# Kernel tuning notes

Hardware: AMD Instinct MI355X
Metric: run time of the kernel (lower is better)

## Reference

```python
import jax, jax.numpy as jnp
import numpy as np

M, IN, OUT = 4096, 4096, 16384

def setup_inputs() -> dict:
    key = jax.random.key(0)
    k1, k2, k3, k4 = jax.random.split(key, 4)
    x = jax.random.normal(k1, (M, IN), dtype=jnp.float32)
    weight = jax.random.randint(k2, (OUT, IN), -127, 127, dtype=jnp.int32).astype(jnp.int8)
    scale = jax.random.uniform(k3, (OUT, 1), dtype=jnp.float32) * 0.01 + 1e-4
    bias = jax.random.normal(k4, (OUT,), dtype=jnp.float32)
    return {"x": x, "weight": weight, "scale": scale, "bias": bias}

def reference(x, weight, scale, bias):
    # Dequantize int8 weights on the fly: [out, in]
    w = weight.astype(x.dtype) * scale
    # F.linear: x @ w.T + bias  -> [M, out]
    return jnp.einsum('mi,oi->mo', x, w) + bias
```

## Files before the change

kernel.cpp:

```cpp
#include <hip/hip_runtime.h>
#include <hip/hip_bf16.h>

#define M_DIM 4096
#define K_DIM 4096
#define N_DIM 16384
#define BM 256
#define BN 256
#define BKB 128
#define NT (K_DIM / BKB)
#define HALF_B 16384
#define BUF_B  (4 * HALF_B)
#define LDS_BYTES (2 * BUF_B)

using i32x4 = __attribute__((ext_vector_type(4))) int;

__global__ void cvt_w_kernel(const int* __restrict__ w,
                             signed char* __restrict__ o, int n) {
    int tid = blockIdx.x * blockDim.x + threadIdx.x;
    int stride = gridDim.x * blockDim.x;
    for (int base = tid * 16; base < n; base += stride * 16) {
        int4 a = *reinterpret_cast<const int4*>(w + base);
        int4 b = *reinterpret_cast<const int4*>(w + base + 4);
        int4 c = *reinterpret_cast<const int4*>(w + base + 8);
        int4 d = *reinterpret_cast<const int4*>(w + base + 12);
        int4 p;
        p.x = (a.x & 255) | ((a.y & 255) << 8) | ((a.z & 255) << 16) | (a.w << 24);
        p.y = (b.x & 255) | ((b.y & 255) << 8) | ((b.z & 255) << 16) | (b.w << 24);
        p.z = (c.x & 255) | ((c.y & 255) << 8) | ((c.z & 255) << 16) | (c.w << 24);
        p.w = (d.x & 255) | ((d.y & 255) << 8) | ((d.z & 255) << 16) | (d.w << 24);
        *reinterpret_cast<int4*>(o + base) = p;
    }
}

__global__ __launch_bounds__(256) void quant_x_kernel(
    const float* __restrict__ x, signed char* __restrict__ q,
    float* __restrict__ xs) {
    int row = blockIdx.x;
    int tid = threadIdx.x;
    const float* xr = x + (size_t)row * K_DIM + tid * 16;
    float4 v0 = *reinterpret_cast<const float4*>(xr + 0);
    float4 v1 = *reinterpret_cast<const float4*>(xr + 4);
    float4 v2 = *reinterpret_cast<const float4*>(xr + 8);
    float4 v3 = *reinterpret_cast<const float4*>(xr + 12);
    float f[16] = {v0.x, v0.y, v0.z, v0.w, v1.x, v1.y, v1.z, v1.w,
                   v2.x, v2.y, v2.z, v2.w, v3.x, v3.y, v3.z, v3.w};
    float m = 0.f;
    #pragma unroll
    for (int i = 0; i < 16; ++i) m = fmaxf(m, fabsf(f[i]));
    #pragma unroll
    for (int off = 32; off > 0; off >>= 1) m = fmaxf(m, __shfl_xor(m, off));
    __shared__ float red[4];
    if ((tid & 63) == 0) red[tid >> 6] = m;
    __syncthreads();
    m = fmaxf(fmaxf(red[0], red[1]), fmaxf(red[2], red[3]));
    float inv = (m > 0.f) ? 127.0f / m : 0.f;
    if (tid == 0) xs[row] = (m > 0.f) ? m / 127.0f : 0.f;
    int b[16];
    #pragma unroll
    for (int i = 0; i < 16; ++i) {
        float t = f[i] * inv;
        t = fminf(fmaxf(t, -127.f), 127.f);
        b[i] = (int)__builtin_rintf(t);
    }
    int4 p;
    p.x = (b[0] & 255) | ((b[1] & 255) << 8) | ((b[2] & 255) << 16) | (b[3] << 24);
    p.y = (b[4] & 255) | ((b[5] & 255) << 8) | ((b[6] & 255) << 16) | (b[7] << 24);
    p.z = (b[8] & 255) | ((b[9] & 255) << 8) | ((b[10] & 255) << 16) | (b[11] << 24);
    p.w = (b[12] & 255) | ((b[13] & 255) << 8) | ((b[14] & 255) << 16) | (b[15] << 24);
    *reinterpret_cast<int4*>(q + (size_t)row * K_DIM + tid * 16) = p;
}

#define FENCE() asm volatile("" ::: "memory")
#define BARRIER() do { FENCE(); __builtin_amdgcn_s_barrier(); FENCE(); } while (0)

#define READ_A(AH)                                                        \
  do { _Pragma("unroll") for (int mi = 0; mi < 4; ++mi) {                 \
    int hr = wm * 64 + mi * 16 + l15;                                     \
    const signed char* hb = lb + (AH) * HALF_B + hr * BKB;                \
    _Pragma("unroll") for (int kk = 0; kk < 2; ++kk)                      \
      af[mi][kk] = *reinterpret_cast<const i32x4*>(                       \
          hb + (((kk * 4 + lg) ^ (hr & 7)) * 16));                        \
  } } while (0)

#define READ_B(DST, BG)                                                   \
  do { _Pragma("unroll") for (int ni = 0; ni < 2; ++ni) {                 \
    int hr = wn * 32 + ni * 16 + l15;                                     \
    const signed char* hb = lb + (2 + (BG)) * HALF_B + hr * BKB;          \
    _Pragma("unroll") for (int kk = 0; kk < 2; ++kk)                      \
      DST[ni][kk] = *reinterpret_cast<const i32x4*>(                      \
          hb + (((kk * 4 + lg) ^ (hr & 7)) * 16));                        \
  } } while (0)

#define MFMA16(BSRC, AH, BG)                                              \
  do { __builtin_amdgcn_s_setprio(1);                                     \
    _Pragma("unroll") for (int kk = 0; kk < 2; ++kk)                      \
      _Pragma("unroll") for (int mi = 0; mi < 4; ++mi)                    \
        _Pragma("unroll") for (int ni = 0; ni < 2; ++ni)                  \
          acc[AH][BG][mi][ni] = __builtin_amdgcn_mfma_i32_16x16x64_i8(    \
              af[mi][kk], BSRC[ni][kk], acc[AH][BG][mi][ni], 0, 0, 0);    \
    __builtin_amdgcn_s_setprio(0);                                        \
  } while (0)

__global__ __launch_bounds__(512, 2) void gemm_kernel(
    const signed char* __restrict__ A,
    const signed char* __restrict__ B,
    const float* __restrict__ scale,
    const float* __restrict__ xs,
    const float* __restrict__ bias,
    float* __restrict__ C)
{
    extern __shared__ signed char lds[];

    const int nwg = (M_DIM / BM) * (N_DIM / BN);
    const int cpx = nwg / 8;
    int bid = blockIdx.x;
    int swz = (bid & 7) * cpx + (bid >> 3);
    const int ntn = N_DIM / BN;
    int tm = swz / ntn;
    int tn = swz % ntn;

    int tid  = threadIdx.x;
    int lane = tid & 63;
    int wid  = tid >> 6;
    int wm   = wid >> 2;
    int wn   = wid & 3;
    int l15  = lane & 15;
    int lg   = lane >> 4;

    const signed char* Ab = A + (size_t)tm * BM * K_DIM;
    const signed char* Bb = B + (size_t)tn * BN * K_DIM;

    auto STAGE = [&](int buf, int half, int t) {
        const signed char* gbase = (half < 2)
            ? Ab + (size_t)(half * 128) * K_DIM
            : Bb + (size_t)((half - 2) * 128) * K_DIM;
        signed char* dbase = lds + buf * BUF_B + half * HALF_B;
        #pragma unroll
        for (int i = 0; i < 2; ++i) {
            int flat = i * 512 + tid;
            int row = flat >> 3, ch = flat & 7;
            const signed char* src =
                gbase + (size_t)row * K_DIM + t * BKB + ((ch ^ (row & 7)) * 16);
            __builtin_amdgcn_global_load_lds(
                (const __attribute__((address_space(1))) unsigned int*)src,
                (__attribute__((address_space(3))) unsigned int*)(dbase + flat * 16),
                16, 0, 0);
        }
    };

    i32x4 acc[2][2][4][2];
    #pragma unroll
    for (int a0 = 0; a0 < 2; ++a0)
      #pragma unroll
      for (int g0 = 0; g0 < 2; ++g0)
        #pragma unroll
        for (int mi = 0; mi < 4; ++mi)
          #pragma unroll
          for (int ni = 0; ni < 2; ++ni)
            acc[a0][g0][mi][ni] = (i32x4){0, 0, 0, 0};

    i32x4 af[4][2], b0[2][2], b1[2][2];

    STAGE(0, 0, 0);
    STAGE(0, 2, 0);
    STAGE(0, 3, 0);
    STAGE(0, 1, 0);
    STAGE(1, 0, 1);
    STAGE(1, 3, 1);
    asm volatile("s_waitcnt vmcnt(4)" ::: "memory");

    for (int t = 0; t < NT; ++t) {
        const signed char* lb = lds + (t & 1) * BUF_B;
        const bool s1 = (t + 1) < NT;
        const bool s2 = (t + 2) < NT;

        BARRIER();
        if (s1) STAGE((t + 1) & 1, 1, t + 1);
        READ_A(0);
        READ_B(b0, 0);
        MFMA16(b0, 0, 0);
        if (s1) STAGE((t + 1) & 1, 2, t + 1);
        READ_B(b1, 1);
        MFMA16(b1, 0, 1);
        BARRIER();
        if (s2) STAGE(t & 1, 0, t + 2);
        READ_A(1);
        MFMA16(b1, 1, 1);
        if (s2) STAGE(t & 1, 3, t + 2);
        MFMA16(b0, 1, 0);
        if (s2) asm volatile("s_waitcnt vmcnt(4)" ::: "memory");
        else    asm volatile("s_waitcnt vmcnt(0)" ::: "memory");
    }

    #pragma unroll
    for (int AH = 0; AH < 2; ++AH)
      #pragma unroll
      for (int BG = 0; BG < 2; ++BG)
        #pragma unroll
        for (int ni = 0; ni < 2; ++ni) {
            int col = tn * BN + BG * 128 + wn * 32 + ni * 16 + l15;
            float s = scale[col];
            float b = bias[col];
            #pragma unroll
            for (int mi = 0; mi < 4; ++mi) {
                int row0 = tm * BM + AH * 128 + wm * 64 + mi * 16 + lg * 4;
                float4 x4 = *reinterpret_cast<const float4*>(xs + row0);
                float xv[4] = {x4.x, x4.y, x4.z, x4.w};
                #pragma unroll
                for (int r = 0; r < 4; ++r)
                    C[(size_t)(row0 + r) * N_DIM + col] =
                        (float)acc[AH][BG][mi][ni][r] * (s * xv[r]) + b;
            }
        }
}

__global__ void naive_kernel(const float* __restrict__ x,
                             const int* __restrict__ w,
                             const float* __restrict__ scale,
                             const float* __restrict__ bias,
                             float* __restrict__ out) {
    long long idx = (long long)blockIdx.x * blockDim.x + threadIdx.x;
    long long total = (long long)M_DIM * N_DIM;
    if (idx >= total) return;
    int m = (int)(idx / N_DIM);
    int o = (int)(idx % N_DIM);
    const float* xr = x + (size_t)m * K_DIM;
    const int* wr = w + (size_t)o * K_DIM;
    float sum = 0.f;
    for (int k = 0; k < K_DIM; ++k) sum += xr[k] * (float)wr[k];
    out[idx] = sum * scale[o] + bias[o];
}

extern "C" void kernel_launch(void* const* d_in, const int* in_sizes, int n_in,
                              void* d_out, int out_size, void* d_ws, size_t ws_size,
                              hipStream_t stream)
{
    const float* x     = (const float*)d_in[0];
    const int*   w     = (const int*)d_in[1];
    const float* scale = (const float*)d_in[2];
    const float* bias  = (const float*)d_in[3];
    float*       out   = (float*)d_out;

    const size_t needW = (size_t)N_DIM * K_DIM;
    const size_t needX = (size_t)M_DIM * K_DIM;
    const size_t needS = (size_t)M_DIM * sizeof(float);

    if (ws_size >= needW + needX + needS) {
        signed char* Wq = (signed char*)d_ws;
        signed char* Xq = (signed char*)((char*)d_ws + needW);
        float*       xs = (float*)((char*)d_ws + needW + needX);
        hipLaunchKernelGGL(cvt_w_kernel, dim3(2048), dim3(256), 0, stream,
                           w, Wq, N_DIM * K_DIM);
        hipLaunchKernelGGL(quant_x_kernel, dim3(M_DIM), dim3(256), 0, stream,
                           x, Xq, xs);
        hipLaunchKernelGGL(gemm_kernel, dim3((M_DIM / BM) * (N_DIM / BN)), dim3(512),
                           LDS_BYTES, stream, Xq, Wq, scale, xs, bias, out);
    } else {
        long long total = (long long)M_DIM * N_DIM;
        int blocks = (int)((total + 255) / 256);
        hipLaunchKernelGGL(naive_kernel, dim3(blocks), dim3(256), 0, stream,
                           x, w, scale, bias, out);
    }
}
```

Baseline: 351.7 us.

## Pre-swizzle weights into MFMA fragment layout and load B directly to registers

The weight conversion kernel now writes int8 weights in a fragment-major layout matching the 16x16x64 MFMA B operand, so each wave loads its B fragments straight from global memory into registers instead of staging through LDS. LDS holds only the A tile now (double buffered), which halves LDS use and removes the B ds_reads. The main loop is restructured into a two-tile unrolled body with register double-buffering of B fragments and a full vmcnt(0) wait plus barrier each tile. The trade-off is that B is no longer shared across waves through LDS, so each wave issues redundant global/L2 reads of B, and the full wait per tile may expose latency.

```diff
diff --git a/kernel.cpp b/kernel.cpp
--- a/kernel.cpp
+++ b/kernel.cpp
@@ -8,28 +8,31 @@
 #define BN 256
 #define BKB 128
 #define NT (K_DIM / BKB)
-#define HALF_B 16384
-#define BUF_B  (4 * HALF_B)
-#define LDS_BYTES (2 * BUF_B)
+#define ATILE_B (BM * BKB)
+#define LDS_BYTES (2 * ATILE_B)
 
 using i32x4 = __attribute__((ext_vector_type(4))) int;
 
-__global__ void cvt_w_kernel(const int* __restrict__ w,
-                             signed char* __restrict__ o, int n) {
-    int tid = blockIdx.x * blockDim.x + threadIdx.x;
-    int stride = gridDim.x * blockDim.x;
-    for (int base = tid * 16; base < n; base += stride * 16) {
-        int4 a = *reinterpret_cast<const int4*>(w + base);
-        int4 b = *reinterpret_cast<const int4*>(w + base + 4);
-        int4 c = *reinterpret_cast<const int4*>(w + base + 8);
-        int4 d = *reinterpret_cast<const int4*>(w + base + 12);
-        int4 p;
-        p.x = (a.x & 255) | ((a.y & 255) << 8) | ((a.z & 255) << 16) | (a.w << 24);
-        p.y = (b.x & 255) | ((b.y & 255) << 8) | ((b.z & 255) << 16) | (b.w << 24);
-        p.z = (c.x & 255) | ((c.y & 255) << 8) | ((c.z & 255) << 16) | (c.w << 24);
-        p.w = (d.x & 255) | ((d.y & 255) << 8) | ((d.z & 255) << 16) | (d.w << 24);
-        *reinterpret_cast<int4*>(o + base) = p;
-    }
+__global__ __launch_bounds__(256) void cvt_w_kernel(
+    const int* __restrict__ w, signed char* __restrict__ o) {
+    int gid  = blockIdx.x * 256 + threadIdx.x;
+    int l    = gid & 63;
+    int frag = gid >> 6;
+    int kt64 = frag & 63;
+    int n16  = frag >> 6;
+    int n = n16 * 16 + (l & 15);
+    int k = kt64 * 64 + (l >> 4) * 16;
+    const int* src = w + (size_t)n * K_DIM + k;
+    int4 a = *reinterpret_cast<const int4*>(src + 0);
+    int4 b = *reinterpret_cast<const int4*>(src + 4);
+    int4 c = *reinterpret_cast<const int4*>(src + 8);
+    int4 d = *reinterpret_cast<const int4*>(src + 12);
+    int4 p;
+    p.x = (a.x & 255) | ((a.y & 255) << 8) | ((a.z & 255) << 16) | (a.w << 24);
+    p.y = (b.x & 255) | ((b.y & 255) << 8) | ((b.z & 255) << 16) | (b.w << 24);
+    p.z = (c.x & 255) | ((c.y & 255) << 8) | ((c.z & 255) << 16) | (c.w << 24);
+    p.w = (d.x & 255) | ((d.y & 255) << 8) | ((d.z & 255) << 16) | (d.w << 24);
+    *reinterpret_cast<int4*>(o + (size_t)gid * 16) = p;
 }
 
 __global__ __launch_bounds__(256) void quant_x_kernel(
@@ -75,35 +78,51 @@
 
 #define READ_A(AH)                                                        \
   do { _Pragma("unroll") for (int mi = 0; mi < 4; ++mi) {                 \
-    int hr = wm * 64 + mi * 16 + l15;                                     \
-    const signed char* hb = lb + (AH) * HALF_B + hr * BKB;                \
+    int hr = (AH) * 128 + wm * 64 + mi * 16 + l15;                        \
+    const signed char* hb = lb + hr * BKB;                                \
     _Pragma("unroll") for (int kk = 0; kk < 2; ++kk)                      \
       af[mi][kk] = *reinterpret_cast<const i32x4*>(                       \
           hb + (((kk * 4 + lg) ^ (hr & 7)) * 16));                        \
   } } while (0)
 
-#define READ_B(DST, BG)                                                   \
-  do { _Pragma("unroll") for (int ni = 0; ni < 2; ++ni) {                 \
-    int hr = wn * 32 + ni * 16 + l15;                                     \
-    const signed char* hb = lb + (2 + (BG)) * HALF_B + hr * BKB;          \
-    _Pragma("unroll") for (int kk = 0; kk < 2; ++kk)                      \
-      DST[ni][kk] = *reinterpret_cast<const i32x4*>(                      \
-          hb + (((kk * 4 + lg) ^ (hr & 7)) * 16));                        \
+#define LOADB(SET, T, KK)                                                 \
+  do { _Pragma("unroll") for (int bg = 0; bg < 2; ++bg)                   \
+    _Pragma("unroll") for (int ni = 0; ni < 2; ++ni) {                    \
+      int n16 = tn * 16 + bg * 8 + wn * 2 + ni;                           \
+      SET[bg][ni] = *reinterpret_cast<const i32x4*>(                      \
+          Bt + (((size_t)(n16 * 64 + (T) * 2 + (KK))) << 10) + lane * 16);\
   } } while (0)
 
-#define MFMA16(BSRC, AH, BG)                                              \
+#define MFMA16(AH, KK, BSET)                                              \
   do { __builtin_amdgcn_s_setprio(1);                                     \
-    _Pragma("unroll") for (int kk = 0; kk < 2; ++kk)                      \
+    _Pragma("unroll") for (int bg = 0; bg < 2; ++bg)                      \
       _Pragma("unroll") for (int mi = 0; mi < 4; ++mi)                    \
         _Pragma("unroll") for (int ni = 0; ni < 2; ++ni)                  \
-          acc[AH][BG][mi][ni] = __builtin_amdgcn_mfma_i32_16x16x64_i8(    \
-              af[mi][kk], BSRC[ni][kk], acc[AH][BG][mi][ni], 0, 0, 0);    \
+          acc[AH][bg][mi][ni] = __builtin_amdgcn_mfma_i32_16x16x64_i8(    \
+              af[mi][KK], BSET[bg][ni], acc[AH][bg][mi][ni], 0, 0, 0);    \
     __builtin_amdgcn_s_setprio(0);                                        \
   } while (0)
 
+#define TILE_BODY(BK0CUR, BK0NXT, T)                                      \
+  {                                                                       \
+    const int s1 = (T) + 1 < NT;                                          \
+    const signed char* lb = lds + ((T) & 1) * ATILE_B;                    \
+    if (s1) STAGE_A(((T) + 1) & 1, (T) + 1);                              \
+    LOADB(bk1, (T), 1);                                                   \
+    if (s1) LOADB(BK0NXT, (T) + 1, 0);                                    \
+    READ_A(0);                                                            \
+    MFMA16(0, 0, BK0CUR);                                                 \
+    MFMA16(0, 1, bk1);                                                    \
+    READ_A(1);                                                            \
+    MFMA16(1, 0, BK0CUR);                                                 \
+    MFMA16(1, 1, bk1);                                                    \
+    asm volatile("s_waitcnt vmcnt(0)" ::: "memory");                      \
+    BARRIER();                                                            \
+  }
+
 __global__ __launch_bounds__(512, 2) void gemm_kernel(
     const signed char* __restrict__ A,
-    const signed char* __restrict__ B,
+    const signed char* __restrict__ Bt,
     const float* __restrict__ scale,
     const float* __restrict__ xs,
     const float* __restrict__ bias,
@@ -128,19 +147,15 @@
     int lg   = lane >> 4;
 
     const signed char* Ab = A + (size_t)tm * BM * K_DIM;
-    const signed char* Bb = B + (size_t)tn * BN * K_DIM;
-
-    auto STAGE = [&](int buf, int half, int t) {
-        const signed char* gbase = (half < 2)
-            ? Ab + (size_t)(half * 128) * K_DIM
-            : Bb + (size_t)((half - 2) * 128) * K_DIM;
-        signed char* dbase = lds + buf * BUF_B + half * HALF_B;
+
+    auto STAGE_A = [&](int buf, int t) {
+        signed char* dbase = lds + buf * ATILE_B;
         #pragma unroll
-        for (int i = 0; i < 2; ++i) {
+        for (int i = 0; i < 4; ++i) {
             int flat = i * 512 + tid;
             int row = flat >> 3, ch = flat & 7;
             const signed char* src =
-                gbase + (size_t)row * K_DIM + t * BKB + ((ch ^ (row & 7)) * 16);
+                Ab + (size_t)row * K_DIM + t * BKB + ((ch ^ (row & 7)) * 16);
             __builtin_amdgcn_global_load_lds(
                 (const __attribute__((address_space(1))) unsigned int*)src,
                 (__attribute__((address_space(3))) unsigned int*)(dbase + flat * 16),
@@ -159,37 +174,16 @@
           for (int ni = 0; ni < 2; ++ni)
             acc[a0][g0][mi][ni] = (i32x4){0, 0, 0, 0};
 
-    i32x4 af[4][2], b0[2][2], b1[2][2];
-
-    STAGE(0, 0, 0);
-    STAGE(0, 2, 0);
-    STAGE(0, 3, 0);
-    STAGE(0, 1, 0);
-    STAGE(1, 0, 1);
-    STAGE(1, 3, 1);
-    asm volatile("s_waitcnt vmcnt(4)" ::: "memory");
-
-    for (int t = 0; t < NT; ++t) {
-        const signed char* lb = lds + (t & 1) * BUF_B;
-        const bool s1 = (t + 1) < NT;
-        const bool s2 = (t + 2) < NT;
-
-        BARRIER();
-        if (s1) STAGE((t + 1) & 1, 1, t + 1);
-        READ_A(0);
-        READ_B(b0, 0);
-        MFMA16(b0, 0, 0);
-        if (s1) STAGE((t + 1) & 1, 2, t + 1);
-        READ_B(b1, 1);
-        MFMA16(b1, 0, 1);
-        BARRIER();
-        if (s2) STAGE(t & 1, 0, t + 2);
-        READ_A(1);
-        MFMA16(b1, 1, 1);
-        if (s2) STAGE(t & 1, 3, t + 2);
-        MFMA16(b0, 1, 0);
-        if (s2) asm volatile("s_waitcnt vmcnt(4)" ::: "memory");
-        else    asm volatile("s_waitcnt vmcnt(0)" ::: "memory");
+    i32x4 af[4][2], bk0A[2][2], bk0B[2][2], bk1[2][2];
+
+    STAGE_A(0, 0);
+    LOADB(bk0A, 0, 0);
+    asm volatile("s_waitcnt vmcnt(0)" ::: "memory");
+    BARRIER();
+
+    for (int tt = 0; tt < NT; tt += 2) {
+        TILE_BODY(bk0A, bk0B, tt);
+        TILE_BODY(bk0B, bk0A, tt + 1);
     }
 
     #pragma unroll
@@ -246,15 +240,15 @@
     const size_t needS = (size_t)M_DIM * sizeof(float);
 
     if (ws_size >= needW + needX + needS) {
-        signed char* Wq = (signed char*)d_ws;
+        signed char* Wt = (signed char*)d_ws;
         signed char* Xq = (signed char*)((char*)d_ws + needW);
         float*       xs = (float*)((char*)d_ws + needW + needX);
-        hipLaunchKernelGGL(cvt_w_kernel, dim3(2048), dim3(256), 0, stream,
-                           w, Wq, N_DIM * K_DIM);
+        hipLaunchKernelGGL(cvt_w_kernel, dim3((N_DIM / 16) * (K_DIM / 64) / 4),
+                           dim3(256), 0, stream, w, Wt);
         hipLaunchKernelGGL(quant_x_kernel, dim3(M_DIM), dim3(256), 0, stream,
                            x, Xq, xs);
         hipLaunchKernelGGL(gemm_kernel, dim3((M_DIM / BM) * (N_DIM / BN)), dim3(512),
-                           LDS_BYTES, stream, Xq, Wq, scale, xs, bias, out);
+                           LDS_BYTES, stream, Xq, Wt, scale, xs, bias, out);
     } else {
         long long total = (long long)M_DIM * N_DIM;
         int blocks = (int)((total + 255) / 256);
```

Result: slower. 523.9 us (+49.0%).

## Use 1024-thread workgroups with 64x64 wave tiles and simple double buffering

Applied to the files above, without the earlier changes.

Restructures the int8 GEMM from 512-thread workgroups (two per CU, each wave owning split 64x32 sub-tiles across halves) to 1024-thread workgroups where each of 16 waves owns a contiguous 64x64 output tile. The staggered half-tile staging schedule with two barriers and partial vmcnt waits is replaced by a plain double-buffered loop: issue the next full tile load, compute on the current one, wait for all loads, then barrier. The aim is simpler code and better register reuse of A/B fragments per MFMA. The cost is losing the fine-grained overlap of loads with compute, and a full-workgroup barrier across 16 waves that can stall MFMA issue.

```diff
diff --git a/kernel.cpp b/kernel.cpp
--- a/kernel.cpp
+++ b/kernel.cpp
@@ -8,9 +8,9 @@
 #define BN 256
 #define BKB 128
 #define NT (K_DIM / BKB)
-#define HALF_B 16384
-#define BUF_B  (4 * HALF_B)
-#define LDS_BYTES (2 * BUF_B)
+#define SLOT_B 16384
+#define TILE_B (4 * SLOT_B)
+#define LDS_BYTES (2 * TILE_B)
 
 using i32x4 = __attribute__((ext_vector_type(4))) int;
 
@@ -73,35 +73,32 @@
 #define FENCE() asm volatile("" ::: "memory")
 #define BARRIER() do { FENCE(); __builtin_amdgcn_s_barrier(); FENCE(); } while (0)
 
-#define READ_A(AH)                                                        \
+#define READ_AK(KK)                                                       \
   do { _Pragma("unroll") for (int mi = 0; mi < 4; ++mi) {                 \
-    int hr = wm * 64 + mi * 16 + l15;                                     \
-    const signed char* hb = lb + (AH) * HALF_B + hr * BKB;                \
-    _Pragma("unroll") for (int kk = 0; kk < 2; ++kk)                      \
-      af[mi][kk] = *reinterpret_cast<const i32x4*>(                       \
-          hb + (((kk * 4 + lg) ^ (hr & 7)) * 16));                        \
+    int hr = (wm & 1) * 64 + mi * 16 + l15;                               \
+    const signed char* hb = lb + (wm >> 1) * SLOT_B + hr * BKB;           \
+    af[mi] = *reinterpret_cast<const i32x4*>(                             \
+        hb + ((((KK) * 4 + lg) ^ (hr & 7)) * 16));                        \
   } } while (0)
 
-#define READ_B(DST, BG)                                                   \
-  do { _Pragma("unroll") for (int ni = 0; ni < 2; ++ni) {                 \
-    int hr = wn * 32 + ni * 16 + l15;                                     \
-    const signed char* hb = lb + (2 + (BG)) * HALF_B + hr * BKB;          \
-    _Pragma("unroll") for (int kk = 0; kk < 2; ++kk)                      \
-      DST[ni][kk] = *reinterpret_cast<const i32x4*>(                      \
-          hb + (((kk * 4 + lg) ^ (hr & 7)) * 16));                        \
+#define READ_BK(KK)                                                       \
+  do { _Pragma("unroll") for (int ni = 0; ni < 4; ++ni) {                 \
+    int hr = (wn & 1) * 64 + ni * 16 + l15;                               \
+    const signed char* hb = lb + (2 + (wn >> 1)) * SLOT_B + hr * BKB;     \
+    bf[ni] = *reinterpret_cast<const i32x4*>(                             \
+        hb + ((((KK) * 4 + lg) ^ (hr & 7)) * 16));                        \
   } } while (0)
 
-#define MFMA16(BSRC, AH, BG)                                              \
+#define MFMA16()                                                          \
   do { __builtin_amdgcn_s_setprio(1);                                     \
-    _Pragma("unroll") for (int kk = 0; kk < 2; ++kk)                      \
-      _Pragma("unroll") for (int mi = 0; mi < 4; ++mi)                    \
-        _Pragma("unroll") for (int ni = 0; ni < 2; ++ni)                  \
-          acc[AH][BG][mi][ni] = __builtin_amdgcn_mfma_i32_16x16x64_i8(    \
-              af[mi][kk], BSRC[ni][kk], acc[AH][BG][mi][ni], 0, 0, 0);    \
+    _Pragma("unroll") for (int mi = 0; mi < 4; ++mi)                      \
+      _Pragma("unroll") for (int ni = 0; ni < 4; ++ni)                    \
+        acc[mi][ni] = __builtin_amdgcn_mfma_i32_16x16x64_i8(              \
+            af[mi], bf[ni], acc[mi][ni], 0, 0, 0);                        \
     __builtin_amdgcn_s_setprio(0);                                        \
   } while (0)
 
-__global__ __launch_bounds__(512, 2) void gemm_kernel(
+__global__ __launch_bounds__(1024) void gemm_kernel(
     const signed char* __restrict__ A,
     const signed char* __restrict__ B,
     const float* __restrict__ scale,
@@ -130,88 +127,64 @@
     const signed char* Ab = A + (size_t)tm * BM * K_DIM;
     const signed char* Bb = B + (size_t)tn * BN * K_DIM;
 
-    auto STAGE = [&](int buf, int half, int t) {
-        const signed char* gbase = (half < 2)
-            ? Ab + (size_t)(half * 128) * K_DIM
-            : Bb + (size_t)((half - 2) * 128) * K_DIM;
-        signed char* dbase = lds + buf * BUF_B + half * HALF_B;
+    int srow = tid >> 3;
+    int sch  = ((tid & 7) ^ (srow & 7)) * 16;
+    auto STAGE = [&](int buf, int t) {
+        signed char* dbase = lds + buf * TILE_B + tid * 16;
         #pragma unroll
-        for (int i = 0; i < 2; ++i) {
-            int flat = i * 512 + tid;
-            int row = flat >> 3, ch = flat & 7;
-            const signed char* src =
-                gbase + (size_t)row * K_DIM + t * BKB + ((ch ^ (row & 7)) * 16);
+        for (int i = 0; i < 4; ++i) {
+            const signed char* src = (i < 2)
+                ? Ab + (size_t)(i * 128 + srow) * K_DIM + t * BKB + sch
+                : Bb + (size_t)((i - 2) * 128 + srow) * K_DIM + t * BKB + sch;
             __builtin_amdgcn_global_load_lds(
                 (const __attribute__((address_space(1))) unsigned int*)src,
-                (__attribute__((address_space(3))) unsigned int*)(dbase + flat * 16),
+                (__attribute__((address_space(3))) unsigned int*)(dbase + i * SLOT_B),
                 16, 0, 0);
         }
     };
 
-    i32x4 acc[2][2][4][2];
-    #pragma unroll
-    for (int a0 = 0; a0 < 2; ++a0)
+    i32x4 acc[4][4];
+    #pragma unroll
+    for (int mi = 0; mi < 4; ++mi)
       #pragma unroll
-      for (int g0 = 0; g0 < 2; ++g0)
+      for (int ni = 0; ni < 4; ++ni)
+        acc[mi][ni] = (i32x4){0, 0, 0, 0};
+
+    i32x4 af[4], bf[4];
+
+    STAGE(0, 0);
+    asm volatile("s_waitcnt vmcnt(0)" ::: "memory");
+    BARRIER();
+
+    for (int t = 0; t < NT; ++t) {
+        const signed char* lb = lds + (t & 1) * TILE_B;
+        if (t + 1 < NT) STAGE((t + 1) & 1, t + 1);
+        READ_AK(0);
+        READ_BK(0);
+        MFMA16();
+        READ_AK(1);
+        READ_BK(1);
+        MFMA16();
+        asm volatile("s_waitcnt vmcnt(0)" ::: "memory");
+        BARRIER();
+    }
+
+    #pragma unroll
+    for (int ni = 0; ni < 4; ++ni) {
+        int col = tn * BN + wn * 64 + ni * 16 + l15;
+        float s = scale[col];
+        float b = bias[col];
         #pragma unroll
-        for (int mi = 0; mi < 4; ++mi)
-          #pragma unroll
-          for (int ni = 0; ni < 2; ++ni)
-            acc[a0][g0][mi][ni] = (i32x4){0, 0, 0, 0};
-
-    i32x4 af[4][2], b0[2][2], b1[2][2];
-
-    STAGE(0, 0, 0);
-    STAGE(0, 2, 0);
-    STAGE(0, 3, 0);
-    STAGE(0, 1, 0);
-    STAGE(1, 0, 1);
-    STAGE(1, 3, 1);
-    asm volatile("s_waitcnt vmcnt(4)" ::: "memory");
-
-    for (int t = 0; t < NT; ++t) {
-        const signed char* lb = lds + (t & 1) * BUF_B;
-        const bool s1 = (t + 1) < NT;
-        const bool s2 = (t + 2) < NT;
-
-        BARRIER();
-        if (s1) STAGE((t + 1) & 1, 1, t + 1);
-        READ_A(0);
-        READ_B(b0, 0);
-        MFMA16(b0, 0, 0);
-        if (s1) STAGE((t + 1) & 1, 2, t + 1);
-        READ_B(b1, 1);
-        MFMA16(b1, 0, 1);
-        BARRIER();
-        if (s2) STAGE(t & 1, 0, t + 2);
-        READ_A(1);
-        MFMA16(b1, 1, 1);
-        if (s2) STAGE(t & 1, 3, t + 2);
-        MFMA16(b0, 1, 0);
-        if (s2) asm volatile("s_waitcnt vmcnt(4)" ::: "memory");
-        else    asm volatile("s_waitcnt vmcnt(0)" ::: "memory");
-    }
-
-    #pragma unroll
-    for (int AH = 0; AH < 2; ++AH)
-      #pragma unroll
-      for (int BG = 0; BG < 2; ++BG)
-        #pragma unroll
-        for (int ni = 0; ni < 2; ++ni) {
-            int col = tn * BN + BG * 128 + wn * 32 + ni * 16 + l15;
-            float s = scale[col];
-            float b = bias[col];
+        for (int mi = 0; mi < 4; ++mi) {
+            int row0 = tm * BM + wm * 64 + mi * 16 + lg * 4;
+            float4 x4 = *reinterpret_cast<const float4*>(xs + row0);
+            float xv[4] = {x4.x, x4.y, x4.z, x4.w};
             #pragma unroll
-            for (int mi = 0; mi < 4; ++mi) {
-                int row0 = tm * BM + AH * 128 + wm * 64 + mi * 16 + lg * 4;
-                float4 x4 = *reinterpret_cast<const float4*>(xs + row0);
-                float xv[4] = {x4.x, x4.y, x4.z, x4.w};
-                #pragma unroll
-                for (int r = 0; r < 4; ++r)
-                    C[(size_t)(row0 + r) * N_DIM + col] =
-                        (float)acc[AH][BG][mi][ni][r] * (s * xv[r]) + b;
-            }
+            for (int r = 0; r < 4; ++r)
+                C[(size_t)(row0 + r) * N_DIM + col] =
+                    (float)acc[mi][ni][r] * (s * xv[r]) + b;
         }
+    }
 }
 
 __global__ void naive_kernel(const float* __restrict__ x,
@@ -253,7 +226,7 @@
                            w, Wq, N_DIM * K_DIM);
         hipLaunchKernelGGL(quant_x_kernel, dim3(M_DIM), dim3(256), 0, stream,
                            x, Xq, xs);
-        hipLaunchKernelGGL(gemm_kernel, dim3((M_DIM / BM) * (N_DIM / BN)), dim3(512),
+        hipLaunchKernelGGL(gemm_kernel, dim3((M_DIM / BM) * (N_DIM / BN)), dim3(1024),
                            LDS_BYTES, stream, Xq, Wq, scale, xs, bias, out);
     } else {
         long long total = (long long)M_DIM * N_DIM;
```

Result: slower. 383.0 us (+8.9%).

## Simplify to single-stage whole-tile prefetch with warp-staggered LDS read order

Applied to the files above, without the earlier changes.

Replaces the fine-grained split-half staging pipeline with a simple double buffer. At the top of each iteration the whole next K-tile (A and B halves) is prefetched, and the loop ends with a full vmcnt(0) wait and a single barrier. Warps in the second M row now walk the sub-tiles in reverse order, which staggers LDS bank accesses and spreads MFMA issue across warps. In exchange it gives up the two-tiles-ahead prefetch depth and the mid-iteration barrier, so global load latency may be exposed more at the end of each iteration.

```diff
diff --git a/kernel.cpp b/kernel.cpp
--- a/kernel.cpp
+++ b/kernel.cpp
@@ -91,7 +91,7 @@
           hb + (((kk * 4 + lg) ^ (hr & 7)) * 16));                        \
   } } while (0)
 
-#define MFMA16(BSRC, AH, BG)                                              \
+#define MFMA16(AH, BG, BSRC)                                              \
   do { __builtin_amdgcn_s_setprio(1);                                     \
     _Pragma("unroll") for (int kk = 0; kk < 2; ++kk)                      \
       _Pragma("unroll") for (int mi = 0; mi < 4; ++mi)                    \
@@ -130,20 +130,22 @@
     const signed char* Ab = A + (size_t)tm * BM * K_DIM;
     const signed char* Bb = B + (size_t)tn * BN * K_DIM;
 
-    auto STAGE = [&](int buf, int half, int t) {
-        const signed char* gbase = (half < 2)
-            ? Ab + (size_t)(half * 128) * K_DIM
-            : Bb + (size_t)((half - 2) * 128) * K_DIM;
-        signed char* dbase = lds + buf * BUF_B + half * HALF_B;
+    auto STAGE = [&](int buf, int t) {
+        signed char* base = lds + buf * BUF_B;
         #pragma unroll
-        for (int i = 0; i < 2; ++i) {
-            int flat = i * 512 + tid;
+        for (int i = 0; i < 8; ++i) {
+            int slot = i >> 1;
+            int flat = (i & 1) * 512 + tid;
             int row = flat >> 3, ch = flat & 7;
-            const signed char* src =
-                gbase + (size_t)row * K_DIM + t * BKB + ((ch ^ (row & 7)) * 16);
+            const signed char* src = (slot < 2)
+                ? Ab + (size_t)(slot * 128 + row) * K_DIM + t * BKB
+                      + ((ch ^ (row & 7)) * 16)
+                : Bb + (size_t)((slot - 2) * 128 + row) * K_DIM + t * BKB
+                      + ((ch ^ (row & 7)) * 16);
             __builtin_amdgcn_global_load_lds(
                 (const __attribute__((address_space(1))) unsigned int*)src,
-                (__attribute__((address_space(3))) unsigned int*)(dbase + flat * 16),
+                (__attribute__((address_space(3))) unsigned int*)
+                    (base + slot * HALF_B + flat * 16),
                 16, 0, 0);
         }
     };
@@ -161,35 +163,36 @@
 
     i32x4 af[4][2], b0[2][2], b1[2][2];
 
-    STAGE(0, 0, 0);
-    STAGE(0, 2, 0);
-    STAGE(0, 3, 0);
-    STAGE(0, 1, 0);
-    STAGE(1, 0, 1);
-    STAGE(1, 3, 1);
-    asm volatile("s_waitcnt vmcnt(4)" ::: "memory");
+    STAGE(0, 0);
+    asm volatile("s_waitcnt vmcnt(0)" ::: "memory");
+    BARRIER();
 
     for (int t = 0; t < NT; ++t) {
         const signed char* lb = lds + (t & 1) * BUF_B;
-        const bool s1 = (t + 1) < NT;
-        const bool s2 = (t + 2) < NT;
-
+        if (t + 1 < NT) STAGE((t + 1) & 1, t + 1);
+
+        if (wm == 0) {
+            READ_A(0);
+            READ_B(b0, 0);
+            MFMA16(0, 0, b0);
+            READ_B(b1, 1);
+            MFMA16(0, 1, b1);
+            READ_A(1);
+            MFMA16(1, 1, b1);
+            MFMA16(1, 0, b0);
+        } else {
+            READ_A(1);
+            READ_B(b1, 1);
+            MFMA16(1, 1, b1);
+            READ_B(b0, 0);
+            MFMA16(1, 0, b0);
+            READ_A(0);
+            MFMA16(0, 0, b0);
+            MFMA16(0, 1, b1);
+        }
+
+        asm volatile("s_waitcnt vmcnt(0)" ::: "memory");
         BARRIER();
-        if (s1) STAGE((t + 1) & 1, 1, t + 1);
-        READ_A(0);
-        READ_B(b0, 0);
-        MFMA16(b0, 0, 0);
-        if (s1) STAGE((t + 1) & 1, 2, t + 1);
-        READ_B(b1, 1);
-        MFMA16(b1, 0, 1);
-        BARRIER();
-        if (s2) STAGE(t & 1, 0, t + 2);
-        READ_A(1);
-        MFMA16(b1, 1, 1);
-        if (s2) STAGE(t & 1, 3, t + 2);
-        MFMA16(b0, 1, 0);
-        if (s2) asm volatile("s_waitcnt vmcnt(4)" ::: "memory");
-        else    asm volatile("s_waitcnt vmcnt(0)" ::: "memory");
     }
 
     #pragma unroll
```

New measurement: 426.1 us. 21.2% more time.
